# Kernel optimization log

Hardware: AMD Instinct MI355X
Metric: run time of the kernel (lower is better)

## Reference

```python
import math
import jax, jax.numpy as jnp
import numpy as np

B, S, D, H, V = 8, 1024, 512, 8, 32000
HD = D // H


def _position_embedding(seq_len, d_model):
    pos = jnp.arange(seq_len, dtype=jnp.float32)[:, None]                 # [S,1]
    div = jnp.exp(jnp.arange(0, d_model, 2, dtype=jnp.float32) * (-math.log(10000.0) / d_model))  # [D/2]
    ang = pos * div                                                        # [S,D/2]
    # interleave sin (even cols) / cos (odd cols)
    return jnp.stack([jnp.sin(ang), jnp.cos(ang)], axis=-1).reshape(seq_len, d_model)


def _min_max_normalize(w):
    lo = jnp.min(w, axis=-1, keepdims=True)
    hi = jnp.max(w, axis=-1, keepdims=True)
    return (w - lo) / (hi - lo)


def _converable_mask(h, Wc, bc):
    bs, seq = h.shape[0], h.shape[1]
    half = seq // 2
    shift = math.ceil(seq / 2)
    width = jnp.einsum('bsd,od->bso', h, Wc)[..., 0] + bc[0]               # [B,S]
    width = _min_max_normalize(width)[..., None]                           # [B,S,1]
    origin = jnp.concatenate([jnp.linspace(1.0, 0.0, half),
                              jnp.linspace(0.0, 1.0, seq - half)])         # [S]
    origin_mask = 1.0 - jax.nn.sigmoid((origin[None, None, :] - width) * 100.0)  # [B,S,S]
    idx = (jnp.arange(seq - 1, -1, -1)[:, None] + jnp.arange(seq)[None, :]) % seq  # [S,S]
    idx = jnp.roll(idx, shift, axis=0)
    # torch.roll of a [1,S] row along dim 0 is a no-op
    cmp = idx >= jnp.arange(seq)[None, :]                                  # [S,S] bool
    move = jnp.concatenate([cmp[:shift], ~cmp[shift:]], axis=0)            # [S,S]
    gathered = jnp.take_along_axis(origin_mask, idx[None, :, :], axis=2)   # [B,S,S]
    return gathered * move.astype(origin_mask.dtype)


def setup_inputs():
    key = jax.random.key(0)
    ks = jax.random.split(key, 9)
    s_emb = 1.0
    s_hd = 1.0 / math.sqrt(HD)
    s_d = 1.0 / math.sqrt(D)
    return {
        'x':   jax.random.randint(ks[0], (B, S), 0, V),
        'emb': jax.random.normal(ks[1], (V, D), dtype=jnp.float32) * s_emb,
        'Wq':  jax.random.normal(ks[2], (HD, HD), dtype=jnp.float32) * s_hd,
        'Wk':  jax.random.normal(ks[3], (HD, HD), dtype=jnp.float32) * s_hd,
        'Wv':  jax.random.normal(ks[4], (HD, HD), dtype=jnp.float32) * s_hd,
        'Wo':  jax.random.normal(ks[5], (D, D), dtype=jnp.float32) * s_d,
        'bo':  jnp.zeros((D,), dtype=jnp.float32),
        'Wc':  jax.random.normal(ks[6], (1, D), dtype=jnp.float32) * s_d,
        'bc':  jnp.zeros((1,), dtype=jnp.float32),
    }


def reference(x, emb, Wq, Wk, Wv, Wo, bo, Wc, bc):
    h = emb[x] + _position_embedding(S, D)[None]                           # [B,S,D]
    mask = _converable_mask(h, Wc, bc)                                     # [B,S,S]
    hh = h.reshape(B, S, H, HD)
    q = jnp.einsum('bshd,od->bsho', hh, Wq)
    k = jnp.einsum('bshd,od->bsho', hh, Wk)
    v = jnp.einsum('bshd,od->bsho', hh, Wv)
    energy = jnp.einsum('bqhd,bkhd->bhqk', q, k)                           # [B,H,S,S]
    # mask [B,S,S] broadcasts as [1,B,S,S]; valid because B == H (as in original)
    energy = energy * mask
    attn = jax.nn.softmax(energy / math.sqrt(D), axis=3)
    out = jnp.einsum('bhqk,bkhd->bqhd', attn, v).reshape(B, S, D)
    out = out @ Wo.T + bo
    return (out, mask)
```

## Files before the change

### kernel.cpp

```cpp
#include <hip/hip_runtime.h>
#include <hip/hip_bf16.h>
#include <math.h>

#define Bn 8
#define Sn 1024
#define Dn 512
#define Hn 8
#define HDn 64

typedef __bf16 bf16x8 __attribute__((ext_vector_type(8)));
typedef __bf16 bf16x4 __attribute__((ext_vector_type(4)));
typedef float  f32x4  __attribute__((ext_vector_type(4)));

__device__ __forceinline__ unsigned enc_f(float v) {
    unsigned u = __float_as_uint(v);
    return (u & 0x80000000u) ? ~u : (u | 0x80000000u);
}
__device__ __forceinline__ float dec_f(unsigned k) {
    unsigned u = (k & 0x80000000u) ? (k ^ 0x80000000u) : ~k;
    return __uint_as_float(u);
}

__global__ __launch_bounds__(256) void k_fused(
        const int* __restrict__ x, const float* __restrict__ emb,
        const float* __restrict__ Wc, const float* __restrict__ bc,
        const float* __restrict__ Wq, const float* __restrict__ Wk,
        const float* __restrict__ Wv,
        float* __restrict__ width, unsigned* __restrict__ lohi,
        __bf16* __restrict__ q, __bf16* __restrict__ k, __bf16* __restrict__ vt) {
    __shared__ __align__(16) __bf16 Xs[64][72];
    __shared__ __align__(16) __bf16 WqS[64][72];
    __shared__ __align__(16) __bf16 WkS[64][72];
    __shared__ __align__(16) __bf16 WvS[64][72];
    __shared__ float wtok[8];
    int t = threadIdx.x;
    int bs0 = blockIdx.x * 8;
    int m0 = blockIdx.x * 64;
    int w = t >> 6, lane = t & 63, quad = lane >> 4, li = lane & 15;

    {
        int token = t >> 5, l32 = t & 31;
        int bs = bs0 + token;
        int s = bs & (Sn - 1);
        int tok = x[bs];
        float wpart = 0.f;
        int row = token * 8 + ((l32 * 16) >> 6);
        #pragma unroll
        for (int j = 0; j < 4; ++j) {
            int d0 = l32 * 16 + j * 4;
            float4 ev = *(const float4*)&emb[(size_t)tok * Dn + d0];
            float4 wc = *(const float4*)&Wc[d0];
            float hv[4];
            #pragma unroll
            for (int i = 0; i < 4; ++i) {
                int d = d0 + i;
                float f = __expf((float)(d & ~1) * (-9.210340371976184f / 512.0f));
                float ang = (float)s * f;
                float pe = (d & 1) ? __cosf(ang) : __sinf(ang);
                hv[i] = (&ev.x)[i] + pe;
                wpart += hv[i] * (&wc.x)[i];
            }
            *(bf16x4*)&Xs[row][d0 & 63] =
                (bf16x4){(__bf16)hv[0], (__bf16)hv[1], (__bf16)hv[2], (__bf16)hv[3]};
        }
        #pragma unroll
        for (int off = 1; off < 32; off <<= 1) wpart += __shfl_xor(wpart, off);
        if (l32 == 0) { float wv = wpart + bc[0]; width[bs] = wv; wtok[token] = wv; }
    }
    #pragma unroll
    for (int it = 0; it < 4; ++it) {
        int e = (it * 256 + t) * 4; int r = e >> 6, c = e & 63;
        float4 qv = *(const float4*)&Wq[e];
        *(bf16x4*)&WqS[r][c] = (bf16x4){(__bf16)qv.x, (__bf16)qv.y, (__bf16)qv.z, (__bf16)qv.w};
        float4 kv = *(const float4*)&Wk[e];
        *(bf16x4*)&WkS[r][c] = (bf16x4){(__bf16)kv.x, (__bf16)kv.y, (__bf16)kv.z, (__bf16)kv.w};
        float4 vv = *(const float4*)&Wv[e];
        *(bf16x4*)&WvS[r][c] = (bf16x4){(__bf16)vv.x, (__bf16)vv.y, (__bf16)vv.z, (__bf16)vv.w};
    }
    __syncthreads();

    if (t == 0) {
        float mn = wtok[0], mx = wtok[0];
        #pragma unroll
        for (int i = 1; i < 8; ++i) { mn = fminf(mn, wtok[i]); mx = fmaxf(mx, wtok[i]); }
        int b = bs0 >> 10;
        atomicMin(&lohi[b], enc_f(mn));
        atomicMin(&lohi[8 + b], ~enc_f(mx));
    }

    bf16x8 A0 = *(const bf16x8*)&Xs[w * 16 + li][quad * 8];
    bf16x8 A1 = *(const bf16x8*)&Xs[w * 16 + li][32 + quad * 8];
    f32x4 aq[4], ak[4], av[4];
    #pragma unroll
    for (int n = 0; n < 4; ++n) {
        aq[n] = (f32x4){0.f,0.f,0.f,0.f}; ak[n] = aq[n]; av[n] = aq[n];
        bf16x8 Bq0 = *(const bf16x8*)&WqS[n * 16 + li][quad * 8];
        bf16x8 Bq1 = *(const bf16x8*)&WqS[n * 16 + li][32 + quad * 8];
        aq[n] = __builtin_amdgcn_mfma_f32_16x16x32_bf16(A0, Bq0, aq[n], 0, 0, 0);
        aq[n] = __builtin_amdgcn_mfma_f32_16x16x32_bf16(A1, Bq1, aq[n], 0, 0, 0);
        bf16x8 Bk0 = *(const bf16x8*)&WkS[n * 16 + li][quad * 8];
        bf16x8 Bk1 = *(const bf16x8*)&WkS[n * 16 + li][32 + quad * 8];
        ak[n] = __builtin_amdgcn_mfma_f32_16x16x32_bf16(A0, Bk0, ak[n], 0, 0, 0);
        ak[n] = __builtin_amdgcn_mfma_f32_16x16x32_bf16(A1, Bk1, ak[n], 0, 0, 0);
        bf16x8 Bv0 = *(const bf16x8*)&WvS[n * 16 + li][quad * 8];
        bf16x8 Bv1 = *(const bf16x8*)&WvS[n * 16 + li][32 + quad * 8];
        av[n] = __builtin_amdgcn_mfma_f32_16x16x32_bf16(A0, Bv0, av[n], 0, 0, 0);
        av[n] = __builtin_amdgcn_mfma_f32_16x16x32_bf16(A1, Bv1, av[n], 0, 0, 0);
    }

    #pragma unroll
    for (int n = 0; n < 4; ++n)
        #pragma unroll
        for (int r = 0; r < 4; ++r) {
            int Rg = m0 + w * 16 + quad * 4 + r;
            int bsI = Rg >> 3, head = Rg & 7;
            int b = bsI >> 10, s = bsI & (Sn - 1);
            size_t oidx = (((size_t)(b * Hn + head)) * Sn + s) * HDn + n * 16 + li;
            q[oidx] = (__bf16)aq[n][r];
            k[oidx] = (__bf16)ak[n][r];
        }

    __bf16 (*Vs)[72] = WqS;
    __syncthreads();
    #pragma unroll
    for (int n = 0; n < 4; ++n)
        #pragma unroll
        for (int r = 0; r < 4; ++r)
            Vs[w * 16 + quad * 4 + r][n * 16 + li] = (__bf16)av[n][r];
    __syncthreads();
    int bs0i = m0 >> 3;
    int b = bs0i >> 10, s0l = bs0i & (Sn - 1);
    #pragma unroll
    for (int i = 0; i < 2; ++i) {
        int p = t + 256 * i;
        int head = p >> 6, o = p & 63;
        __bf16 tmp[8];
        #pragma unroll
        for (int j = 0; j < 8; ++j) tmp[j] = Vs[j * 8 + head][o];
        *(bf16x8*)&vt[(((size_t)(b * Hn + head)) * HDn + o) * Sn + s0l] = *(bf16x8*)tmp;
    }
}

__global__ void k_mask(const float* __restrict__ width, const unsigned* __restrict__ lohi,
                       float* __restrict__ mask_out, __bf16* __restrict__ maskb) {
    const float SCALE = 0.04419417382415922f;
    int bs = blockIdx.x;
    int b = bs >> 10;
    int s = bs & (Sn - 1);
    float lo = dec_f(lohi[b]);
    float hi = dec_f(~lohi[8 + b]);
    float wn = (width[bs] - lo) / (hi - lo);
    for (int t = threadIdx.x; t < Sn; t += 256) {
        int it = (t - s + 1535) & (Sn - 1);
        float origin = (it < 512) ? (1.0f - (float)it * (1.0f / 511.0f))
                                  : ((float)(it - 512) * (1.0f / 511.0f));
        float z = (origin - wn) * 100.0f;
        float om;
        if (z >= 0.0f) { float e = __expf(-z); om = e / (1.0f + e); }
        else           { float e = __expf(z);  om = 1.0f / (1.0f + e); }
        bool cmpv = (it >= t);
        bool mv = (s < 512) ? cmpv : !cmpv;
        float val = mv ? om : 0.0f;
        mask_out[(size_t)bs * Sn + t] = val;
        maskb[(size_t)bs * Sn + t] = (__bf16)(val * SCALE);
    }
}

__global__ __launch_bounds__(256) void k_attn(
        const __bf16* __restrict__ q, const __bf16* __restrict__ k,
        const __bf16* __restrict__ vt, const __bf16* __restrict__ maskb,
        __bf16* __restrict__ ao) {
    __shared__ __align__(16) __bf16 Ks[64][72];
    __shared__ __align__(16) __bf16 Vt[64][72];
    __shared__ __align__(16) __bf16 Ps[64][76];
    int blk = blockIdx.x;
    int hh = blk & 7;
    int qt = (blk >> 3) & 15;
    int b  = blk >> 7;
    int bh = b * Hn + hh;
    int q0 = qt * 64;
    int t = threadIdx.x;
    int w = t >> 6, lane = t & 63, quad = lane >> 4, li = lane & 15;

    const __bf16* qbase  = q  + ((size_t)bh * Sn + q0) * HDn;
    const __bf16* kbase  = k  + (size_t)bh * Sn * HDn;
    const __bf16* vtbase = vt + (size_t)bh * HDn * Sn;
    const __bf16* mrow[4];
    #pragma unroll
    for (int r = 0; r < 4; ++r)
        mrow[r] = maskb + ((size_t)hh * Sn + q0 + w * 16 + quad * 4 + r) * Sn;

    bf16x8 A0 = *(const bf16x8*)&qbase[(w * 16 + li) * HDn + quad * 8];
    bf16x8 A1 = *(const bf16x8*)&qbase[(w * 16 + li) * HDn + 32 + quad * 8];

    bf16x8 pk[2], pv[2];
    #pragma unroll
    for (int it = 0; it < 2; ++it) {
        int e = (it * 256 + t) * 8; int r = e >> 6, c = e & 63;
        pk[it] = *(const bf16x8*)&kbase[e];
        pv[it] = *(const bf16x8*)&vtbase[(size_t)r * Sn + c];
    }

    f32x4 O[4];
    #pragma unroll
    for (int n = 0; n < 4; ++n) O[n] = (f32x4){0.f, 0.f, 0.f, 0.f};
    float rs[4] = {0.f, 0.f, 0.f, 0.f};

    for (int k0 = 0; k0 < Sn; k0 += 64) {
        if (k0) __syncthreads();
        #pragma unroll
        for (int it = 0; it < 2; ++it) {
            int e = (it * 256 + t) * 8; int r = e >> 6, c = e & 63;
            *(bf16x8*)&Ks[r][c] = pk[it];
            *(bf16x8*)&Vt[r][c] = pv[it];
        }
        __syncthreads();
        if (k0 + 64 < Sn) {
            #pragma unroll
            for (int it = 0; it < 2; ++it) {
                int e = (it * 256 + t) * 8; int r = e >> 6, c = e & 63;
                pk[it] = *(const bf16x8*)&kbase[(size_t)(k0 + 64) * HDn + e];
                pv[it] = *(const bf16x8*)&vtbase[(size_t)r * Sn + (k0 + 64) + c];
            }
        }

        float msk[4][4];
        #pragma unroll
        for (int n = 0; n < 4; ++n)
            #pragma unroll
            for (int r = 0; r < 4; ++r)
                msk[n][r] = (float)mrow[r][k0 + n * 16 + li];

        f32x4 Sf[4];
        #pragma unroll
        for (int n = 0; n < 4; ++n) {
            f32x4 acc = (f32x4){0.f, 0.f, 0.f, 0.f};
            bf16x8 B0 = *(const bf16x8*)&Ks[n * 16 + li][quad * 8];
            acc = __builtin_amdgcn_mfma_f32_16x16x32_bf16(A0, B0, acc, 0, 0, 0);
            bf16x8 B1 = *(const bf16x8*)&Ks[n * 16 + li][32 + quad * 8];
            acc = __builtin_amdgcn_mfma_f32_16x16x32_bf16(A1, B1, acc, 0, 0, 0);
            Sf[n] = acc;
        }

        #pragma unroll
        for (int n = 0; n < 4; ++n)
            #pragma unroll
            for (int r = 0; r < 4; ++r) {
                float p = __expf(Sf[n][r] * msk[n][r]);
                rs[r] += p;
                Ps[w * 16 + quad * 4 + r][n * 16 + li] = (__bf16)p;
            }

        #pragma unroll
        for (int kc = 0; kc < 2; ++kc) {
            bf16x8 Ap = *(const bf16x8*)&Ps[w * 16 + li][kc * 32 + quad * 8];
            #pragma unroll
            for (int n = 0; n < 4; ++n) {
                bf16x8 Bv = *(const bf16x8*)&Vt[n * 16 + li][kc * 32 + quad * 8];
                O[n] = __builtin_amdgcn_mfma_f32_16x16x32_bf16(Ap, Bv, O[n], 0, 0, 0);
            }
        }
    }

    #pragma unroll
    for (int off = 1; off < 16; off <<= 1)
        #pragma unroll
        for (int r = 0; r < 4; ++r) rs[r] += __shfl_xor(rs[r], off);
    float inv[4];
    #pragma unroll
    for (int r = 0; r < 4; ++r) inv[r] = __fdividef(1.0f, rs[r]);
    #pragma unroll
    for (int n = 0; n < 4; ++n)
        #pragma unroll
        for (int r = 0; r < 4; ++r)
            ao[((size_t)b * Sn + q0 + w * 16 + quad * 4 + r) * Dn + hh * HDn + n * 16 + li]
                = (__bf16)(O[n][r] * inv[r]);
}

__global__ __launch_bounds__(256) void k_proj(
        const __bf16* __restrict__ ao, const float* __restrict__ Wo,
        const float* __restrict__ bo, float* __restrict__ out) {
    __shared__ __align__(16) __bf16 As[64][72];
    __shared__ __align__(16) __bf16 Bs[64][72];
    int bm = blockIdx.x >> 3;
    int bn = blockIdx.x & 7;
    int m0 = bm * 64, n0 = bn * 64;
    int t = threadIdx.x;
    int w = t >> 6, lane = t & 63, quad = lane >> 4, li = lane & 15;

    f32x4 O[4];
    #pragma unroll
    for (int n = 0; n < 4; ++n) O[n] = (f32x4){0.f, 0.f, 0.f, 0.f};

    for (int k0 = 0; k0 < Dn; k0 += 64) {
        if (k0) __syncthreads();
        #pragma unroll
        for (int it = 0; it < 2; ++it) {
            int e = (it * 256 + t) * 8; int r = e >> 6, c = e & 63;
            *(bf16x8*)&As[r][c] = *(const bf16x8*)&ao[(size_t)(m0 + r) * Dn + k0 + c];
        }
        #pragma unroll
        for (int it = 0; it < 4; ++it) {
            int e = (it * 256 + t) * 4; int r = e >> 6, c = e & 63;
            float4 wv = *(const float4*)&Wo[(size_t)(n0 + r) * Dn + k0 + c];
            *(bf16x4*)&Bs[r][c] = (bf16x4){(__bf16)wv.x, (__bf16)wv.y, (__bf16)wv.z, (__bf16)wv.w};
        }
        __syncthreads();

        bf16x8 A0 = *(const bf16x8*)&As[w * 16 + li][quad * 8];
        bf16x8 A1 = *(const bf16x8*)&As[w * 16 + li][32 + quad * 8];
        #pragma unroll
        for (int n = 0; n < 4; ++n) {
            bf16x8 B0 = *(const bf16x8*)&Bs[n * 16 + li][quad * 8];
            O[n] = __builtin_amdgcn_mfma_f32_16x16x32_bf16(A0, B0, O[n], 0, 0, 0);
            bf16x8 B1 = *(const bf16x8*)&Bs[n * 16 + li][32 + quad * 8];
            O[n] = __builtin_amdgcn_mfma_f32_16x16x32_bf16(A1, B1, O[n], 0, 0, 0);
        }
    }

    #pragma unroll
    for (int n = 0; n < 4; ++n) {
        float bias = bo[n0 + n * 16 + li];
        #pragma unroll
        for (int r = 0; r < 4; ++r)
            out[(size_t)(m0 + w * 16 + quad * 4 + r) * Dn + n0 + n * 16 + li] = O[n][r] + bias;
    }
}

extern "C" void kernel_launch(void* const* d_in, const int* in_sizes, int n_in,
                              void* d_out, int out_size, void* d_ws, size_t ws_size,
                              hipStream_t stream) {
    const int*   x   = (const int*)d_in[0];
    const float* emb = (const float*)d_in[1];
    const float* Wq  = (const float*)d_in[2];
    const float* Wk  = (const float*)d_in[3];
    const float* Wv  = (const float*)d_in[4];
    const float* Wo  = (const float*)d_in[5];
    const float* bo  = (const float*)d_in[6];
    const float* Wc  = (const float*)d_in[7];
    const float* bc  = (const float*)d_in[8];

    float* ws      = (float*)d_ws;
    float* width   = ws;
    unsigned* lohi = (unsigned*)(width + Bn * Sn);
    __bf16* qb   = (__bf16*)(ws + Bn * Sn + 16);
    __bf16* kb   = qb + (size_t)Bn * Sn * Dn;
    __bf16* vtb  = kb + (size_t)Bn * Sn * Dn;
    __bf16* maskb = vtb + (size_t)Bn * Sn * Dn;
    __bf16* ao   = maskb + (size_t)Bn * Sn * Sn;

    float* out      = (float*)d_out;
    float* mask_out = out + (size_t)Bn * Sn * Dn;

    hipMemsetAsync(lohi, 0xFF, 16 * sizeof(unsigned), stream);
    k_fused<<<(Bn * Sn) / 8, 256, 0, stream>>>(x, emb, Wc, bc, Wq, Wk, Wv,
                                               width, lohi, qb, kb, vtb);
    k_mask<<<Bn * Sn, 256, 0, stream>>>(width, lohi, mask_out, maskb);
    k_attn<<<Bn * Hn * (Sn / 64), 256, 0, stream>>>(qb, kb, vtb, maskb, ao);
    k_proj<<<(Bn * Sn / 64) * (Dn / 64), 256, 0, stream>>>(ao, Wo, bo, out);
}
```

Before: 207.7 us.

## Restructure attention kernel with 32x32 MFMA, register-resident P, double-buffered K/V

The attention kernel switches from 16x16x32 to 32x32x16 MFMA, computing S transposed (K as the A operand) so the probabilities stay in registers. A lane-swap shuffle rearranges them into the B operand of the PV MFMA, which removes the shared-memory P round trip. Each block now handles 128 query rows (32 per wave) with double-buffered K/V tiles, one barrier per tile, setprio around MFMA phases and launch bounds requesting 2 blocks per SM. This halves the number of blocks, to 512, and increases register pressure. Mask loads become vectorized bf16x4 reads.

```diff
diff --git a/kernel.cpp b/kernel.cpp
--- a/kernel.cpp
+++ b/kernel.cpp
@@ -10,7 +10,10 @@
 
 typedef __bf16 bf16x8 __attribute__((ext_vector_type(8)));
 typedef __bf16 bf16x4 __attribute__((ext_vector_type(4)));
+typedef __bf16 bf16x2 __attribute__((ext_vector_type(2)));
 typedef float  f32x4  __attribute__((ext_vector_type(4)));
+typedef float  f32x16 __attribute__((ext_vector_type(16)));
+typedef unsigned int u32x4 __attribute__((ext_vector_type(4)));
 
 __device__ __forceinline__ unsigned enc_f(float v) {
     unsigned u = __float_as_uint(v);
@@ -166,115 +169,142 @@
     }
 }
 
-__global__ __launch_bounds__(256) void k_attn(
+__global__ __launch_bounds__(256, 2) void k_attn(
         const __bf16* __restrict__ q, const __bf16* __restrict__ k,
         const __bf16* __restrict__ vt, const __bf16* __restrict__ maskb,
         __bf16* __restrict__ ao) {
-    __shared__ __align__(16) __bf16 Ks[64][72];
-    __shared__ __align__(16) __bf16 Vt[64][72];
-    __shared__ __align__(16) __bf16 Ps[64][76];
+    __shared__ __align__(16) __bf16 Ks[2][64][72];
+    __shared__ __align__(16) __bf16 Vt[2][64][72];
     int blk = blockIdx.x;
     int hh = blk & 7;
-    int qt = (blk >> 3) & 15;
-    int b  = blk >> 7;
+    int qt = (blk >> 3) & 7;
+    int b  = blk >> 6;
     int bh = b * Hn + hh;
-    int q0 = qt * 64;
+    int q0 = qt * 128;
     int t = threadIdx.x;
-    int w = t >> 6, lane = t & 63, quad = lane >> 4, li = lane & 15;
-
-    const __bf16* qbase  = q  + ((size_t)bh * Sn + q0) * HDn;
+    int w = t >> 6, lane = t & 63, hi5 = lane >> 5, l31 = lane & 31;
+
+    const __bf16* qbase  = q  + ((size_t)bh * Sn + q0 + w * 32) * HDn;
     const __bf16* kbase  = k  + (size_t)bh * Sn * HDn;
     const __bf16* vtbase = vt + (size_t)bh * HDn * Sn;
-    const __bf16* mrow[4];
-    #pragma unroll
-    for (int r = 0; r < 4; ++r)
-        mrow[r] = maskb + ((size_t)hh * Sn + q0 + w * 16 + quad * 4 + r) * Sn;
-
-    bf16x8 A0 = *(const bf16x8*)&qbase[(w * 16 + li) * HDn + quad * 8];
-    bf16x8 A1 = *(const bf16x8*)&qbase[(w * 16 + li) * HDn + 32 + quad * 8];
-
-    bf16x8 pk[2], pv[2];
-    #pragma unroll
-    for (int it = 0; it < 2; ++it) {
-        int e = (it * 256 + t) * 8; int r = e >> 6, c = e & 63;
-        pk[it] = *(const bf16x8*)&kbase[e];
-        pv[it] = *(const bf16x8*)&vtbase[(size_t)r * Sn + c];
-    }
-
-    f32x4 O[4];
-    #pragma unroll
-    for (int n = 0; n < 4; ++n) O[n] = (f32x4){0.f, 0.f, 0.f, 0.f};
-    float rs[4] = {0.f, 0.f, 0.f, 0.f};
-
-    for (int k0 = 0; k0 < Sn; k0 += 64) {
-        if (k0) __syncthreads();
-        #pragma unroll
-        for (int it = 0; it < 2; ++it) {
-            int e = (it * 256 + t) * 8; int r = e >> 6, c = e & 63;
-            *(bf16x8*)&Ks[r][c] = pk[it];
-            *(bf16x8*)&Vt[r][c] = pv[it];
-        }
-        __syncthreads();
-        if (k0 + 64 < Sn) {
+    const __bf16* mq = maskb + ((size_t)hh * Sn + q0 + w * 32 + l31) * Sn;
+
+    bf16x8 Qf[4];
+    #pragma unroll
+    for (int c = 0; c < 4; ++c)
+        Qf[c] = *(const bf16x8*)&qbase[(size_t)l31 * HDn + c * 16 + hi5 * 8];
+
+    int sr0 = t >> 3, sc0 = (t & 7) * 8;
+    bf16x8 pk0, pk1, pv0, pv1;
+    pk0 = *(const bf16x8*)&kbase[(size_t)sr0 * HDn + sc0];
+    pk1 = *(const bf16x8*)&kbase[(size_t)(sr0 + 32) * HDn + sc0];
+    pv0 = *(const bf16x8*)&vtbase[(size_t)sr0 * Sn + sc0];
+    pv1 = *(const bf16x8*)&vtbase[(size_t)(sr0 + 32) * Sn + sc0];
+    *(bf16x8*)&Ks[0][sr0][sc0] = pk0;
+    *(bf16x8*)&Ks[0][sr0 + 32][sc0] = pk1;
+    *(bf16x8*)&Vt[0][sr0][sc0] = pv0;
+    *(bf16x8*)&Vt[0][sr0 + 32][sc0] = pv1;
+    __syncthreads();
+
+    f32x16 OT[2];
+    OT[0] = (f32x16){0.f,0.f,0.f,0.f,0.f,0.f,0.f,0.f,0.f,0.f,0.f,0.f,0.f,0.f,0.f,0.f};
+    OT[1] = OT[0];
+    float rs = 0.f;
+
+    for (int ti = 0; ti < 16; ++ti) {
+        int cur = ti & 1;
+
+        bf16x4 mk[2][4];
+        #pragma unroll
+        for (int kg = 0; kg < 2; ++kg)
             #pragma unroll
-            for (int it = 0; it < 2; ++it) {
-                int e = (it * 256 + t) * 8; int r = e >> 6, c = e & 63;
-                pk[it] = *(const bf16x8*)&kbase[(size_t)(k0 + 64) * HDn + e];
-                pv[it] = *(const bf16x8*)&vtbase[(size_t)r * Sn + (k0 + 64) + c];
+            for (int g = 0; g < 4; ++g)
+                mk[kg][g] = *(const bf16x4*)&mq[ti * 64 + kg * 32 + g * 8 + hi5 * 4];
+
+        if (ti < 15) {
+            int k0n = (ti + 1) * 64;
+            pk0 = *(const bf16x8*)&kbase[(size_t)(k0n + sr0) * HDn + sc0];
+            pk1 = *(const bf16x8*)&kbase[(size_t)(k0n + sr0 + 32) * HDn + sc0];
+            pv0 = *(const bf16x8*)&vtbase[(size_t)sr0 * Sn + k0n + sc0];
+            pv1 = *(const bf16x8*)&vtbase[(size_t)(sr0 + 32) * Sn + k0n + sc0];
+        }
+
+        f32x16 St[2];
+        St[0] = (f32x16){0.f,0.f,0.f,0.f,0.f,0.f,0.f,0.f,0.f,0.f,0.f,0.f,0.f,0.f,0.f,0.f};
+        St[1] = St[0];
+        __builtin_amdgcn_s_setprio(1);
+        #pragma unroll
+        for (int c = 0; c < 4; ++c) {
+            bf16x8 K0 = *(const bf16x8*)&Ks[cur][l31][c * 16 + hi5 * 8];
+            St[0] = __builtin_amdgcn_mfma_f32_32x32x16_bf16(K0, Qf[c], St[0], 0, 0, 0);
+            bf16x8 K1 = *(const bf16x8*)&Ks[cur][32 + l31][c * 16 + hi5 * 8];
+            St[1] = __builtin_amdgcn_mfma_f32_32x32x16_bf16(K1, Qf[c], St[1], 0, 0, 0);
+        }
+        __builtin_amdgcn_s_setprio(0);
+
+        unsigned pkd[2][4][2];
+        #pragma unroll
+        for (int kg = 0; kg < 2; ++kg) {
+            #pragma unroll
+            for (int g = 0; g < 4; ++g) {
+                float p0 = __expf(St[kg][4 * g + 0] * (float)mk[kg][g][0]);
+                float p1 = __expf(St[kg][4 * g + 1] * (float)mk[kg][g][1]);
+                float p2 = __expf(St[kg][4 * g + 2] * (float)mk[kg][g][2]);
+                float p3 = __expf(St[kg][4 * g + 3] * (float)mk[kg][g][3]);
+                rs += (p0 + p1) + (p2 + p3);
+                bf16x2 plo = { (__bf16)p0, (__bf16)p1 };
+                bf16x2 phi = { (__bf16)p2, (__bf16)p3 };
+                pkd[kg][g][0] = __builtin_bit_cast(unsigned, plo);
+                pkd[kg][g][1] = __builtin_bit_cast(unsigned, phi);
             }
         }
 
-        float msk[4][4];
-        #pragma unroll
-        for (int n = 0; n < 4; ++n)
-            #pragma unroll
-            for (int r = 0; r < 4; ++r)
-                msk[n][r] = (float)mrow[r][k0 + n * 16 + li];
-
-        f32x4 Sf[4];
-        #pragma unroll
-        for (int n = 0; n < 4; ++n) {
-            f32x4 acc = (f32x4){0.f, 0.f, 0.f, 0.f};
-            bf16x8 B0 = *(const bf16x8*)&Ks[n * 16 + li][quad * 8];
-            acc = __builtin_amdgcn_mfma_f32_16x16x32_bf16(A0, B0, acc, 0, 0, 0);
-            bf16x8 B1 = *(const bf16x8*)&Ks[n * 16 + li][32 + quad * 8];
-            acc = __builtin_amdgcn_mfma_f32_16x16x32_bf16(A1, B1, acc, 0, 0, 0);
-            Sf[n] = acc;
-        }
-
-        #pragma unroll
-        for (int n = 0; n < 4; ++n)
-            #pragma unroll
-            for (int r = 0; r < 4; ++r) {
-                float p = __expf(Sf[n][r] * msk[n][r]);
-                rs[r] += p;
-                Ps[w * 16 + quad * 4 + r][n * 16 + li] = (__bf16)p;
-            }
-
-        #pragma unroll
-        for (int kc = 0; kc < 2; ++kc) {
-            bf16x8 Ap = *(const bf16x8*)&Ps[w * 16 + li][kc * 32 + quad * 8];
-            #pragma unroll
-            for (int n = 0; n < 4; ++n) {
-                bf16x8 Bv = *(const bf16x8*)&Vt[n * 16 + li][kc * 32 + quad * 8];
-                O[n] = __builtin_amdgcn_mfma_f32_16x16x32_bf16(Ap, Bv, O[n], 0, 0, 0);
-            }
-        }
-    }
-
-    #pragma unroll
-    for (int off = 1; off < 16; off <<= 1)
-        #pragma unroll
-        for (int r = 0; r < 4; ++r) rs[r] += __shfl_xor(rs[r], off);
-    float inv[4];
-    #pragma unroll
-    for (int r = 0; r < 4; ++r) inv[r] = __fdividef(1.0f, rs[r]);
-    #pragma unroll
-    for (int n = 0; n < 4; ++n)
-        #pragma unroll
-        for (int r = 0; r < 4; ++r)
-            ao[((size_t)b * Sn + q0 + w * 16 + quad * 4 + r) * Dn + hh * HDn + n * 16 + li]
-                = (__bf16)(O[n][r] * inv[r]);
+        __builtin_amdgcn_s_setprio(1);
+        #pragma unroll
+        for (int c = 0; c < 4; ++c) {
+            const int kg = c >> 1, gA = 2 * (c & 1), gB = gA + 1;
+            unsigned z0 = hi5 ? pkd[kg][gB][0] : pkd[kg][gA][0];
+            unsigned z1 = hi5 ? pkd[kg][gB][1] : pkd[kg][gA][1];
+            unsigned y0 = hi5 ? pkd[kg][gA][0] : pkd[kg][gB][0];
+            unsigned y1 = hi5 ? pkd[kg][gA][1] : pkd[kg][gB][1];
+            unsigned x0 = (unsigned)__shfl_xor((int)y0, 32);
+            unsigned x1 = (unsigned)__shfl_xor((int)y1, 32);
+            u32x4 du;
+            du[0] = hi5 ? x0 : z0;
+            du[1] = hi5 ? x1 : z1;
+            du[2] = hi5 ? z0 : x0;
+            du[3] = hi5 ? z1 : x1;
+            bf16x8 Pf = __builtin_bit_cast(bf16x8, du);
+            bf16x8 V0 = *(const bf16x8*)&Vt[cur][l31][c * 16 + hi5 * 8];
+            OT[0] = __builtin_amdgcn_mfma_f32_32x32x16_bf16(V0, Pf, OT[0], 0, 0, 0);
+            bf16x8 V1 = *(const bf16x8*)&Vt[cur][32 + l31][c * 16 + hi5 * 8];
+            OT[1] = __builtin_amdgcn_mfma_f32_32x32x16_bf16(V1, Pf, OT[1], 0, 0, 0);
+        }
+        __builtin_amdgcn_s_setprio(0);
+
+        if (ti < 15) {
+            *(bf16x8*)&Ks[cur ^ 1][sr0][sc0] = pk0;
+            *(bf16x8*)&Ks[cur ^ 1][sr0 + 32][sc0] = pk1;
+            *(bf16x8*)&Vt[cur ^ 1][sr0][sc0] = pv0;
+            *(bf16x8*)&Vt[cur ^ 1][sr0 + 32][sc0] = pv1;
+            __syncthreads();
+        }
+    }
+
+    rs += __shfl_xor(rs, 32);
+    float inv = __fdividef(1.0f, rs);
+
+    size_t orow = ((size_t)b * Sn + q0 + w * 32 + l31) * Dn + hh * HDn;
+    #pragma unroll
+    for (int og = 0; og < 2; ++og)
+        #pragma unroll
+        for (int g2 = 0; g2 < 4; ++g2) {
+            bf16x4 ov = { (__bf16)(OT[og][4 * g2 + 0] * inv),
+                          (__bf16)(OT[og][4 * g2 + 1] * inv),
+                          (__bf16)(OT[og][4 * g2 + 2] * inv),
+                          (__bf16)(OT[og][4 * g2 + 3] * inv) };
+            *(bf16x4*)&ao[orow + og * 32 + g2 * 8 + hi5 * 4] = ov;
+        }
 }
 
 __global__ __launch_bounds__(256) void k_proj(
@@ -356,6 +386,6 @@
     k_fused<<<(Bn * Sn) / 8, 256, 0, stream>>>(x, emb, Wc, bc, Wq, Wk, Wv,
                                                width, lohi, qb, kb, vtb);
     k_mask<<<Bn * Sn, 256, 0, stream>>>(width, lohi, mask_out, maskb);
-    k_attn<<<Bn * Hn * (Sn / 64), 256, 0, stream>>>(qb, kb, vtb, maskb, ao);
+    k_attn<<<Bn * Hn * (Sn / 128), 256, 0, stream>>>(qb, kb, vtb, maskb, ao);
     k_proj<<<(Bn * Sn / 64) * (Dn / 64), 256, 0, stream>>>(ao, Wo, bo, out);
 }
```

Result: no change. 208.1 us (+0.2%).
